# Kernel optimization log

Measured on AMD Instinct MI355X. Metric: run time of the kernel, lower is better.

Reference implementation:

```python
import jax, jax.numpy as jnp
import numpy as np

N_NODES = 100_000
N_EDGES = 1_000_000
D_X = 8
H = 128
N_DOM = 32768
N_BND = 8192
RE = 1.0 / 1.45e-05  # Reynolds number used in momentum residuals


def setup_inputs() -> dict:
    key = jax.random.key(0)
    ks = jax.random.split(key, 16)
    s = 0.05
    return {
        "x": jax.random.normal(ks[0], (N_NODES, D_X), jnp.float32),
        "x_mask": jax.random.uniform(ks[1], (N_NODES, 6), dtype=jnp.float32),
        "edge_index": jax.random.randint(ks[2], (2, N_EDGES), 0, N_NODES),
        "edge_attr": jax.random.normal(ks[3], (N_EDGES, 4), jnp.float32),
        "pos": jax.random.normal(ks[4], (N_NODES, 3), jnp.float32),
        "batch": jnp.zeros((N_NODES,), jnp.int32),
        "domain_sampling_points": jax.random.normal(ks[5], (N_DOM, 2), jnp.float32),
        "boundary_sampling_points": jax.random.normal(ks[6], (N_BND, 2), jnp.float32),
        "idxs_boundary_sampled": jax.random.randint(ks[7], (N_BND,), 0, N_NODES),
        # surrogate net parameters
        "Wx": jax.random.normal(ks[8], (D_X, H), jnp.float32) * s,
        "Wp": jax.random.normal(ks[9], (2, H), jnp.float32) * s,
        "We": jax.random.normal(ks[10], (3, H), jnp.float32) * s,
        "Wout": jax.random.normal(ks[11], (H, 3), jnp.float32) * s,
        "W1": jax.random.normal(ks[12], (2 + H, H), jnp.float32) * s,
        "b1": jnp.zeros((H,), jnp.float32),
        "W2": jax.random.normal(ks[13], (H, H), jnp.float32) * s,
        "b2": jnp.zeros((H,), jnp.float32),
        "W3": jax.random.normal(ks[14], (H, 3), jnp.float32) * s,
    }


def reference(x, x_mask, edge_index, edge_attr, pos, batch,
              domain_sampling_points, boundary_sampling_points,
              idxs_boundary_sampled,
              Wx, Wp, We, Wout, W1, b1, W2, b2, W3):
    pos2 = pos[:, :2]                              # pos = pos[:, :2]
    ea = edge_attr[:, jnp.array([0, 1, 3])]        # edge_attr[:, [0,1,3]]

    # --- surrogate GNN: one message-passing layer -> supervised output ---
    node_h = jnp.tanh(x @ Wx + pos2 @ Wp)          # [N, H]
    src, dst = edge_index[0], edge_index[1]
    msg = node_h[src] * (ea @ We)                  # [E, H] large gather (memory-bound)
    agg = jax.ops.segment_sum(msg, dst, num_segments=node_h.shape[0])
    h = jnp.tanh(node_h + agg)                     # [N, H]
    out_sup = h @ Wout                             # [N, 3]
    ctx = h.mean(axis=0)                           # [H] pooled graph context (constant wrt sp)

    # --- per-point coordinate network (u, v, p) ---
    def f_samp(sp):
        z = jnp.concatenate([sp, ctx])
        h1 = jnp.tanh(z @ W1 + b1)
        h2 = jnp.tanh(h1 @ W2 + b2)
        return h2 @ W3                             # [3] -> (u, v, p)

    sp = jnp.concatenate([domain_sampling_points, boundary_sampling_points])  # [S, 2]
    out_samp = jax.vmap(f_samp)(sp)                            # [S, 3]
    grads = jax.vmap(jax.jacrev(f_samp))(sp)                   # [S, 3, 2]
    hess = jax.vmap(jax.jacrev(jax.jacrev(f_samp)))(sp)        # [S, 3, 2, 2]

    nd = domain_sampling_points.shape[0]
    # --- domain (full_laminar) residuals ---
    u, v = out_samp[:nd, 0], out_samp[:nd, 1]
    u_x, u_y = grads[:nd, 0, 0], grads[:nd, 0, 1]
    v_x, v_y = grads[:nd, 1, 0], grads[:nd, 1, 1]
    p_x, p_y = grads[:nd, 2, 0], grads[:nd, 2, 1]
    u_xx, u_yy = hess[:nd, 0, 0, 0], hess[:nd, 0, 1, 1]
    v_xx, v_yy = hess[:nd, 1, 0, 0], hess[:nd, 1, 1, 1]
    continuity = u_x + v_y
    momentum_x = u * u_x + v * u_y + p_x - (u_xx + u_yy) / RE
    momentum_y = u * v_x + v * v_y + p_y - (v_xx + v_yy) / RE

    # --- boundary-condition residuals (vmapped BC math) ---
    bu, bv, bp = out_samp[nd:, 0], out_samp[nd:, 1], out_samp[nd:, 2]
    bu_x, bv_y = grads[nd:, 0, 0], grads[nd:, 1, 1]
    bp_x, bp_y = grads[nd:, 2, 0], grads[nd:, 2, 1]
    x_BC = x[idxs_boundary_sampled]                # [B, D_X]
    m = x_mask[idxs_boundary_sampled]              # [B, 6]
    t_x, t_y = x_BC[:, 0], x_BC[:, 1]
    n_x, n_y = -t_y, t_x
    r_vt = jnp.abs(t_x * bu + t_y * bv - x_BC[:, 2]) * m[:, 1]
    r_vn = jnp.abs(n_x * bu + n_y * bv - x_BC[:, 3]) * m[:, 2]
    r_p = jnp.abs(bp - x_BC[:, 4]) * m[:, 3]
    r_dvdn = jnp.abs(n_x * bu_x + n_y * bv_y - x_BC[:, 5]) * m[:, 4]
    r_dpdn = jnp.abs(n_x * bp_x + n_y * bp_y - x_BC[:, 6]) * m[:, 5]
    c = m[:, 1:6].sum(axis=1)
    boundary = (r_vt + r_vn + r_p + r_dvdn + r_dpdn) / c

    return (out_sup, continuity, momentum_x, momentum_y, boundary)
```

## Files before the change

kernel.cpp:

```cpp
#include <hip/hip_runtime.h>
#include <hip/hip_fp8.h>
#include <math.h>

#define H 128
#define DXI 8
#define NNODES 100000
#define NEDGES 1000000
#define NRUNS (NEDGES / 64)
#define NDOM 32768
#define NBND 8192
#define NPTS (NDOM + NBND)
#define INV_RE 1.45e-05f
#define NODE_BLOCKS 1024
#define NPR (NNODES / 8)

#define NSB ((NNODES + 1023) / 1024)

#define CONT_OFF (NNODES * 3)
#define MOMX_OFF (CONT_OFF + NDOM)
#define MOMY_OFF (MOMX_OFF + NDOM)
#define BND_OFF  (MOMY_OFF + NDOM)

#define KPAD 136
#define A_STRIDE (32 * KPAD)

typedef __attribute__((ext_vector_type(8))) short short8;
typedef __attribute__((ext_vector_type(4))) float f32x4;

__device__ __forceinline__ float fast_tanh(float x) {
    const float e = __builtin_amdgcn_exp2f(x * 2.88539008f);
    return fmaf(-2.f, __builtin_amdgcn_rcpf(e + 1.f), 1.f);
}

__device__ __forceinline__ unsigned pack_bf16(float a, float b) {
    unsigned ua = __float_as_uint(a), ub = __float_as_uint(b);
    ua += 0x7fffu + ((ua >> 16) & 1u);
    ub += 0x7fffu + ((ub >> 16) & 1u);
    return (ua >> 16) | (ub & 0xffff0000u);
}

__device__ __forceinline__ short to_bf16(float f) {
    unsigned u = __float_as_uint(f);
    u += 0x7fffu + ((u >> 16) & 1u);
    return (short)(u >> 16);
}

__device__ __forceinline__ float fp8_dec(unsigned b) {
    __hip_fp8_e4m3 d;
    d.__x = (__hip_fp8_storage_t)b;
    return (float)d;
}

__global__ __launch_bounds__(256) void hist_kernel(
    const int* __restrict__ eidx, int* __restrict__ counts)
{
    const int* dst = eidx + NEDGES;
    for (int e = blockIdx.x * 256 + threadIdx.x; e < NEDGES; e += gridDim.x * 256)
        atomicAdd(&counts[dst[e]], 1);
}

__global__ __launch_bounds__(256) void scan1_kernel(
    const int* __restrict__ counts, int* __restrict__ excl, int* __restrict__ bsum,
    const float* __restrict__ x, const float* __restrict__ pos,
    const float* __restrict__ Wx, const float* __restrict__ Wp,
    unsigned short* __restrict__ th, uint4* __restrict__ agg4)
{
    const int tid = threadIdx.x;

    if (blockIdx.x < NSB) {
        const int b = blockIdx.x;
        const int base = b * 1024 + tid * 4;
        int v0 = 0, v1 = 0, v2 = 0, v3 = 0;
        if (base + 3 < NNODES) {
            const int4 t = *(const int4*)(counts + base);
            v0 = t.x; v1 = t.y; v2 = t.z; v3 = t.w;
        } else {
            if (base     < NNODES) v0 = counts[base];
            if (base + 1 < NNODES) v1 = counts[base + 1];
            if (base + 2 < NNODES) v2 = counts[base + 2];
            if (base + 3 < NNODES) v3 = counts[base + 3];
        }
        const int own = v0 + v1 + v2 + v3;
        int s = own;
        const int lane = tid & 63, wv = tid >> 6;
#pragma unroll
        for (int d = 1; d < 64; d <<= 1) {
            const int t = __shfl_up(s, d);
            if (lane >= d) s += t;
        }
        __shared__ int wsum[4];
        if (lane == 63) wsum[wv] = s;
        __syncthreads();
        int woff = 0;
        for (int w = 0; w < wv; ++w) woff += wsum[w];
        const int e0 = s - own + woff;
        const int e1 = e0 + v0, e2 = e1 + v1, e3 = e2 + v2;
        if (base + 3 < NNODES) {
            *(int4*)(excl + base) = make_int4(e0, e1, e2, e3);
        } else {
            if (base     < NNODES) excl[base]     = e0;
            if (base + 1 < NNODES) excl[base + 1] = e1;
            if (base + 2 < NNODES) excl[base + 2] = e2;
            if (base + 3 < NNODES) excl[base + 3] = e3;
        }
        if (tid == 0) bsum[b] = wsum[0] + wsum[1] + wsum[2] + wsum[3];
    }

    const int gid = blockIdx.x * 256 + tid;
    const uint4 z = make_uint4(0u, 0u, 0u, 0u);
    for (size_t i = gid; i < (size_t)NNODES * 16; i += (size_t)gridDim.x * 256)
        agg4[i] = z;

    const int lane = tid & 63;
    const int wv   = tid >> 6;
    const int c0 = lane * 2, c1 = c0 + 1;
    float wxa[DXI], wxb_[DXI];
#pragma unroll
    for (int k = 0; k < DXI; ++k) { wxa[k] = Wx[k * H + c0]; wxb_[k] = Wx[k * H + c1]; }
    const float wp00 = Wp[c0], wp01 = Wp[H + c0];
    const float wp10 = Wp[c1], wp11 = Wp[H + c1];

    for (int n = blockIdx.x * 4 + wv; n < NNODES; n += gridDim.x * 4) {
        const float* xr = x + (size_t)n * DXI;
        const float px = pos[(size_t)n * 3], py = pos[(size_t)n * 3 + 1];
        float a0 = fmaf(wp00, px, wp01 * py);
        float a1 = fmaf(wp10, px, wp11 * py);
#pragma unroll
        for (int k = 0; k < DXI; ++k) {
            const float xv = xr[k];
            a0 = fmaf(xv, wxa[k], a0);
            a1 = fmaf(xv, wxb_[k], a1);
        }
        const __hip_fp8_e4m3 q0(fast_tanh(a0));
        const __hip_fp8_e4m3 q1(fast_tanh(a1));
        th[(size_t)n * 64 + lane] =
            (unsigned short)((unsigned)q0.__x | ((unsigned)q1.__x << 8));
    }
}

__global__ __launch_bounds__(128) void scan2_kernel(int* __restrict__ bsum)
{
    const int tid = threadIdx.x;
    int v = (tid < NSB) ? bsum[tid] : 0;
    const int own = v;
    const int lane = tid & 63, wv = tid >> 6;
#pragma unroll
    for (int d = 1; d < 64; d <<= 1) {
        const int t = __shfl_up(v, d);
        if (lane >= d) v += t;
    }
    __shared__ int ws2[2];
    if (lane == 63) ws2[wv] = v;
    __syncthreads();
    if (wv == 1) v += ws2[0];
    if (tid < NSB) bsum[tid] = v - own;
}

__global__ __launch_bounds__(256) void scan3_kernel(
    int* __restrict__ offsets, int* __restrict__ cursor, const int* __restrict__ bsum)
{
    const int tid = threadIdx.x, b = blockIdx.x;
    const int base = b * 1024 + tid * 4;
    const int add = bsum[b];
    if (base + 3 < NNODES) {
        int4 t = *(const int4*)(offsets + base);
        t.x += add; t.y += add; t.z += add; t.w += add;
        *(int4*)(offsets + base) = t;
        *(int4*)(cursor + base) = t;
    } else {
        for (int i = 0; i < 4; ++i)
            if (base + i < NNODES) {
                const int t = offsets[base + i] + add;
                offsets[base + i] = t;
                cursor[base + i] = t;
            }
    }
}

__global__ __launch_bounds__(256) void scatter_kernel(
    const int* __restrict__ eidx, const float* __restrict__ eattr,
    int* __restrict__ cursor, uint2* __restrict__ csrE)
{
    const int* dst = eidx + NEDGES;
    const int G   = gridDim.x >> 3;
    const int g   = blockIdx.x >> 3;
    const int r   = blockIdx.x & 7;
    const int dlo = r * NPR, dhi = dlo + NPR;
    for (int e = g * 256 + threadIdx.x; e < NEDGES; e += G * 256) {
        const int d = dst[e];
        if (d >= dlo && d < dhi) {
            const float4 ea = ((const float4*)eattr)[e];
            const int slot = atomicAdd(&cursor[d], 1);
            const __hip_fp8_e4m3 f0(ea.x), f1(ea.y), f3(ea.w);
            const unsigned long long v =
                (unsigned long long)(unsigned)eidx[e]
              | ((unsigned long long)(unsigned)d << 17)
              | ((unsigned long long)f0.__x << 34)
              | ((unsigned long long)f1.__x << 42)
              | ((unsigned long long)f3.__x << 50);
            csrE[slot] = make_uint2((unsigned)v, (unsigned)(v >> 32));
        }
    }
}

__global__ __launch_bounds__(256) void seg_edge_kernel(
    const uint2* __restrict__ csrE, const unsigned short* __restrict__ th,
    const float* __restrict__ We, unsigned* __restrict__ agg)
{
    const int run = blockIdx.x * 4 + (threadIdx.x >> 6);
    if (run >= NRUNS) return;
    const int lane = threadIdx.x & 63;
    const int c0 = lane * 2, c1 = c0 + 1;

    const float wea0 = We[c0], wea1 = We[H + c0], wea2 = We[2 * H + c0];
    const float web0 = We[c1], web1 = We[H + c1], web2 = We[2 * H + c1];

    const uint2 rec = csrE[(size_t)run * 64 + lane];
    const int mysrc = (int)(rec.x & 0x1FFFFu);
    const int mydst = (int)((rec.x >> 17) | ((rec.y & 3u) << 15));

    float acc0 = 0.f, acc1 = 0.f;
    bool first = true;
    int cur = __builtin_amdgcn_readlane(mydst, 0);

#pragma unroll
    for (int sub = 0; sub < 4; ++sub) {
        unsigned short rowv[16];
#pragma unroll
        for (int t = 0; t < 16; ++t) {
            const int s = __builtin_amdgcn_readlane(mysrc, sub * 16 + t);
            rowv[t] = th[(size_t)s * 64 + lane];
        }
#pragma unroll
        for (int t = 0; t < 16; ++t) {
            const int e = sub * 16 + t;
            const unsigned hi = (unsigned)__builtin_amdgcn_readlane((int)rec.y, e);
            const float e0f = fp8_dec((hi >> 2) & 0xffu);
            const float e1f = fp8_dec((hi >> 10) & 0xffu);
            const float e3f = fp8_dec((hi >> 18) & 0xffu);
            const float th0 = fp8_dec(rowv[t] & 0xffu);
            const float th1 = fp8_dec((unsigned)rowv[t] >> 8);
            const float w0 = fmaf(e0f, wea0, fmaf(e1f, wea1, e3f * wea2));
            const float w1 = fmaf(e0f, web0, fmaf(e1f, web1, e3f * web2));
            acc0 = fmaf(th0, w0, acc0);
            acc1 = fmaf(th1, w1, acc1);

            const int nxt = (e < 63) ? __builtin_amdgcn_readlane(mydst, e + 1) : -1;
            if (nxt != cur) {
                unsigned* p = agg + (size_t)cur * 64 + lane;
                if (first || e == 63) {
                    unsigned old = *p;
                    while (true) {
                        const float g0 = __uint_as_float(old << 16) + acc0;
                        const float g1 = __uint_as_float(old & 0xffff0000u) + acc1;
                        const unsigned nw = pack_bf16(g0, g1);
                        const unsigned prev = atomicCAS(p, old, nw);
                        if (prev == old) break;
                        old = prev;
                    }
                } else {
                    *p = pack_bf16(acc0, acc1);
                }
                acc0 = 0.f; acc1 = 0.f;
                first = false;
                cur = nxt;
            }
        }
    }
}

__global__ __launch_bounds__(256) void node_kernel(
    const float* __restrict__ x, const float* __restrict__ pos,
    const unsigned* __restrict__ agg,
    const float* __restrict__ Wx, const float* __restrict__ Wp,
    const float* __restrict__ Wout,
    float* __restrict__ out_sup, float* __restrict__ ctx_part)
{
    const int lane = threadIdx.x & 63;
    const int wv   = threadIdx.x >> 6;
    const int c0 = lane * 2, c1 = c0 + 1;

    float wxa[DXI], wxb_[DXI];
#pragma unroll
    for (int k = 0; k < DXI; ++k) { wxa[k] = Wx[k * H + c0]; wxb_[k] = Wx[k * H + c1]; }
    const float wp00 = Wp[c0], wp01 = Wp[H + c0];
    const float wp10 = Wp[c1], wp11 = Wp[H + c1];
    const float woa0 = Wout[c0 * 3], woa1 = Wout[c0 * 3 + 1], woa2 = Wout[c0 * 3 + 2];
    const float wob0 = Wout[c1 * 3], wob1 = Wout[c1 * 3 + 1], wob2 = Wout[c1 * 3 + 2];

    float ctx0 = 0.f, ctx1 = 0.f;

    for (int n = blockIdx.x * 4 + wv; n < NNODES; n += gridDim.x * 4) {
        const unsigned ag = agg[(size_t)n * 64 + lane];
        const float* xr = x + (size_t)n * DXI;
        const float px = pos[(size_t)n * 3], py = pos[(size_t)n * 3 + 1];
        float a0 = fmaf(wp00, px, wp01 * py);
        float a1 = fmaf(wp10, px, wp11 * py);
#pragma unroll
        for (int k = 0; k < DXI; ++k) {
            const float xv = xr[k];
            a0 = fmaf(xv, wxa[k], a0);
            a1 = fmaf(xv, wxb_[k], a1);
        }
        const float h0 = fast_tanh(fast_tanh(a0) + __uint_as_float(ag << 16));
        const float h1 = fast_tanh(fast_tanh(a1) + __uint_as_float(ag & 0xffff0000u));
        ctx0 += h0; ctx1 += h1;

        float p0 = fmaf(h0, woa0, h1 * wob0);
        float p1 = fmaf(h0, woa1, h1 * wob1);
        float p2 = fmaf(h0, woa2, h1 * wob2);
#pragma unroll
        for (int m = 32; m; m >>= 1) {
            p0 += __shfl_xor(p0, m);
            p1 += __shfl_xor(p1, m);
            p2 += __shfl_xor(p2, m);
        }
        if (lane == 0) {
            out_sup[(size_t)n * 3 + 0] = p0;
            out_sup[(size_t)n * 3 + 1] = p1;
            out_sup[(size_t)n * 3 + 2] = p2;
        }
    }

    __shared__ float part[4][H];
    part[wv][c0] = ctx0;
    part[wv][c1] = ctx1;
    __syncthreads();
    if (threadIdx.x < H) {
        const int ch = threadIdx.x;
        ctx_part[(size_t)blockIdx.x * H + ch] =
            part[0][ch] + part[1][ch] + part[2][ch] + part[3][ch];
    }
}

__global__ __launch_bounds__(128) void ctx_kernel(
    const float* __restrict__ ctx_part, const float* __restrict__ W1,
    const float* __restrict__ b1, float* __restrict__ tab)
{
    __shared__ float ctx[H];
    const int ch = threadIdx.x;
    float s0 = 0.f, s1 = 0.f, s2 = 0.f, s3 = 0.f;
#pragma unroll 4
    for (int b = 0; b < NODE_BLOCKS; b += 4) {
        s0 += ctx_part[(size_t)(b + 0) * H + ch];
        s1 += ctx_part[(size_t)(b + 1) * H + ch];
        s2 += ctx_part[(size_t)(b + 2) * H + ch];
        s3 += ctx_part[(size_t)(b + 3) * H + ch];
    }
    ctx[ch] = (s0 + s1 + s2 + s3) * (1.0f / (float)NNODES);
    __syncthreads();
    float acc = b1[ch];
    for (int k = 0; k < H; ++k) acc = fmaf(ctx[k], W1[(size_t)(2 + k) * H + ch], acc);
    const float A0 = W1[ch], A1 = W1[H + ch];
    tab[ch * 8 + 0] = A0;
    tab[ch * 8 + 1] = A1;
    tab[ch * 8 + 2] = acc;
    tab[ch * 8 + 3] = A0 * A0;
    tab[ch * 8 + 4] = A1 * A1;
    tab[ch * 8 + 5] = 0.f;
    tab[ch * 8 + 6] = 0.f;
    tab[ch * 8 + 7] = 0.f;
}

__global__ __launch_bounds__(256, 2) void samp_mfma_kernel(
    const float* __restrict__ dom, const float* __restrict__ bnd,
    const int* __restrict__ bidx,
    const float* __restrict__ x, const float* __restrict__ xmask,
    const float* __restrict__ tab,
    const float* __restrict__ W2, const float* __restrict__ b2,
    const float* __restrict__ W3, float* __restrict__ out)
{
    __shared__ __attribute__((aligned(16))) short Bt[128 * KPAD];
    __shared__ __attribute__((aligned(16))) short Alds[5 * A_STRIDE];
    __shared__ __attribute__((aligned(16))) float red[32][13];

    const int tid = threadIdx.x;
    const int blk = blockIdx.x;

    for (int i = tid; i < H * H; i += 256) {
        const int k = i >> 7, n = i & 127;
        Bt[n * KPAD + k] = to_bf16(W2[i]);
    }

    for (int idx = tid; idx < 32 * 64; idx += 256) {
        const int pl = idx >> 6;
        const int k0 = (idx & 63) * 2;
        const int p  = blk * 32 + pl;
        float spx, spy;
        if (p < NDOM) { spx = dom[(size_t)p * 2];          spy = dom[(size_t)p * 2 + 1]; }
        else          { spx = bnd[(size_t)(p - NDOM) * 2]; spy = bnd[(size_t)(p - NDOM) * 2 + 1]; }
        float v[2][5];
#pragma unroll
        for (int kk = 0; kk < 2; ++kk) {
            const int k = k0 + kk;
            const float4 t4 = *(const float4*)(tab + (size_t)k * 8);
            const float A1s = tab[(size_t)k * 8 + 4];
            const float A0 = t4.x, A1 = t4.y, cc = t4.z, A0s = t4.w;
            const float a1 = fmaf(spx, A0, fmaf(spy, A1, cc));
            const float e  = __builtin_amdgcn_exp2f(a1 * 2.88539008f);
            const float h1 = fmaf(-2.f, __builtin_amdgcn_rcpf(e + 1.f), 1.f);
            const float t1 = fmaf(-h1, h1, 1.f);
            const float m2 = -2.f * h1 * t1;
            v[kk][0] = h1;
            v[kk][1] = t1 * A0;
            v[kk][2] = t1 * A1;
            v[kk][3] = m2 * A0s;
            v[kk][4] = m2 * A1s;
        }
        const int base = pl * KPAD + k0;
#pragma unroll
        for (int q = 0; q < 5; ++q)
            *(unsigned*)&Alds[q * A_STRIDE + base] = pack_bf16(v[0][q], v[1][q]);
    }
    __syncthreads();

    const int lane = tid & 63;
    const int wv = tid >> 6;
    const int pt = wv >> 1;
    const int jh = wv & 1;
    const int ln = lane & 15;
    const int hi = lane >> 4;

    f32x4 acc[4][5];
#pragma unroll
    for (int nt = 0; nt < 4; ++nt)
#pragma unroll
        for (int q = 0; q < 5; ++q)
            acc[nt][q] = (f32x4){0.f, 0.f, 0.f, 0.f};

#pragma unroll
    for (int kc = 0; kc < 4; ++kc) {
        short8 af[5];
#pragma unroll
        for (int q = 0; q < 5; ++q)
            af[q] = *(const short8*)&Alds[q * A_STRIDE + (pt * 16 + ln) * KPAD + kc * 32 + hi * 8];
        short8 bfr[4];
#pragma unroll
        for (int nt = 0; nt < 4; ++nt)
            bfr[nt] = *(const short8*)&Bt[(jh * 64 + nt * 16 + ln) * KPAD + kc * 32 + hi * 8];
#pragma unroll
        for (int nt = 0; nt < 4; ++nt)
#pragma unroll
            for (int q = 0; q < 5; ++q)
                acc[nt][q] = __builtin_amdgcn_mfma_f32_16x16x32_bf16(af[q], bfr[nt], acc[nt][q], 0, 0, 0);
    }

    float w30[4], w31[4], w32[4], b2j[4];
#pragma unroll
    for (int nt = 0; nt < 4; ++nt) {
        const int j = jh * 64 + nt * 16 + ln;
        w30[nt] = W3[j * 3];
        w31[nt] = W3[j * 3 + 1];
        w32[nt] = W3[j * 3 + 2];
        b2j[nt] = b2[j];
    }

    float rr[4][13];
#pragma unroll
    for (int i = 0; i < 4; ++i)
#pragma unroll
        for (int c = 0; c < 13; ++c) rr[i][c] = 0.f;

#pragma unroll
    for (int i = 0; i < 4; ++i) {
#pragma unroll
        for (int nt = 0; nt < 4; ++nt) {
            const float a2v  = acc[nt][0][i] + b2j[nt];
            const float d2xv = acc[nt][1][i];
            const float d2yv = acc[nt][2][i];
            const float exxv = acc[nt][3][i];
            const float eyyv = acc[nt][4][i];
            const float h2 = fast_tanh(a2v);
            const float t2 = fmaf(-h2, h2, 1.f);
            const float gx = t2 * d2xv;
            const float gy = t2 * d2yv;
            const float hxx = fmaf(-2.f * h2 * gx, d2xv, t2 * exxv);
            const float hyy = fmaf(-2.f * h2 * gy, d2yv, t2 * eyyv);
            rr[i][0]  = fmaf(h2, w30[nt], rr[i][0]);
            rr[i][1]  = fmaf(h2, w31[nt], rr[i][1]);
            rr[i][2]  = fmaf(h2, w32[nt], rr[i][2]);
            rr[i][3]  = fmaf(gx, w30[nt], rr[i][3]);
            rr[i][4]  = fmaf(gx, w31[nt], rr[i][4]);
            rr[i][5]  = fmaf(gx, w32[nt], rr[i][5]);
            rr[i][6]  = fmaf(gy, w30[nt], rr[i][6]);
            rr[i][7]  = fmaf(gy, w31[nt], rr[i][7]);
            rr[i][8]  = fmaf(gy, w32[nt], rr[i][8]);
            rr[i][9]  = fmaf(hxx, w30[nt], rr[i][9]);
            rr[i][10] = fmaf(hxx, w31[nt], rr[i][10]);
            rr[i][11] = fmaf(hyy, w30[nt], rr[i][11]);
            rr[i][12] = fmaf(hyy, w31[nt], rr[i][12]);
        }
    }

#pragma unroll
    for (int m = 1; m < 16; m <<= 1)
#pragma unroll
        for (int i = 0; i < 4; ++i)
#pragma unroll
            for (int c = 0; c < 13; ++c)
                rr[i][c] += __shfl_xor(rr[i][c], m);

    if (ln == 0 && jh == 0) {
#pragma unroll
        for (int i = 0; i < 4; ++i) {
            const int pl = pt * 16 + hi * 4 + i;
#pragma unroll
            for (int c = 0; c < 13; ++c) red[pl][c] = rr[i][c];
        }
    }
    __syncthreads();
    if (ln == 0 && jh == 1) {
#pragma unroll
        for (int i = 0; i < 4; ++i) {
            const int pl = pt * 16 + hi * 4 + i;
#pragma unroll
            for (int c = 0; c < 13; ++c) red[pl][c] += rr[i][c];
        }
    }
    __syncthreads();

    if (tid < 32) {
        const int p = blk * 32 + tid;
        float s[13];
#pragma unroll
        for (int c = 0; c < 13; ++c) s[c] = red[tid][c];
        const float u = s[0], v = s[1], pp = s[2];
        const float ux = s[3], vx = s[4], px = s[5];
        const float uy = s[6], vy = s[7], py = s[8];
        const float uxx = s[9], vxx = s[10], uyy = s[11], vyy = s[12];
        if (p < NDOM) {
            out[CONT_OFF + p] = ux + vy;
            out[MOMX_OFF + p] = fmaf(u, ux, fmaf(v, uy, px)) - (uxx + uyy) * INV_RE;
            out[MOMY_OFF + p] = fmaf(u, vx, fmaf(v, vy, py)) - (vxx + vyy) * INV_RE;
        } else {
            const int i = p - NDOM;
            const int idx = bidx[i];
            const float* xbp = x + (size_t)idx * DXI;
            const float* mm = xmask + (size_t)idx * 6;
            const float tx = xbp[0], ty = xbp[1];
            const float nx = -ty, ny = tx;
            const float r_vt = fabsf(tx * u + ty * v - xbp[2]) * mm[1];
            const float r_vn = fabsf(nx * u + ny * v - xbp[3]) * mm[2];
            const float r_p  = fabsf(pp - xbp[4]) * mm[3];
            const float r_dv = fabsf(nx * ux + ny * vy - xbp[5]) * mm[4];
            const float r_dp = fabsf(nx * px + ny * py - xbp[6]) * mm[5];
            const float c = mm[1] + mm[2] + mm[3] + mm[4] + mm[5];
            out[BND_OFF + i] = (r_vt + r_vn + r_p + r_dv + r_dp) / c;
        }
    }
}

extern "C" void kernel_launch(void* const* d_in, const int* in_sizes, int n_in,
                              void* d_out, int out_size, void* d_ws, size_t ws_size,
                              hipStream_t stream) {
    const float* x     = (const float*)d_in[0];
    const float* xmask = (const float*)d_in[1];
    const int*   eidx  = (const int*)d_in[2];
    const float* eattr = (const float*)d_in[3];
    const float* pos   = (const float*)d_in[4];
    const float* dom   = (const float*)d_in[6];
    const float* bnd   = (const float*)d_in[7];
    const int*   bidx  = (const int*)d_in[8];
    const float* Wx    = (const float*)d_in[9];
    const float* Wp    = (const float*)d_in[10];
    const float* We    = (const float*)d_in[11];
    const float* Wout  = (const float*)d_in[12];
    const float* W1    = (const float*)d_in[13];
    const float* b1    = (const float*)d_in[14];
    const float* W2    = (const float*)d_in[15];
    const float* b2    = (const float*)d_in[16];
    const float* W3    = (const float*)d_in[17];

    float* out = (float*)d_out;

    int*            counts   = (int*)d_ws;
    int*            offsets  = counts + NNODES;
    int*            cursor   = offsets + NNODES + 8;
    int*            bsum     = cursor + NNODES;
    uint2*          csrE     = (uint2*)(bsum + 128);
    unsigned short* th       = (unsigned short*)(csrE + NEDGES);
    unsigned*       agg      = (unsigned*)(th + (size_t)NNODES * 64);
    float*          ctx_part = (float*)(agg + (size_t)NNODES * 64);
    float*          tab      = ctx_part + (size_t)NODE_BLOCKS * H;

    (void)hipMemsetAsync(counts, 0, (size_t)NNODES * sizeof(int), stream);

    hist_kernel<<<1024, 256, 0, stream>>>(eidx, counts);
    scan1_kernel<<<2048, 256, 0, stream>>>(counts, offsets, bsum, x, pos, Wx, Wp, th, (uint4*)agg);
    scan2_kernel<<<1, 128, 0, stream>>>(bsum);
    scan3_kernel<<<NSB, 256, 0, stream>>>(offsets, cursor, bsum);
    scatter_kernel<<<8192, 256, 0, stream>>>(eidx, eattr, cursor, csrE);
    seg_edge_kernel<<<(NRUNS + 3) / 4, 256, 0, stream>>>(csrE, th, We, agg);
    node_kernel<<<NODE_BLOCKS, 256, 0, stream>>>(x, pos, agg, Wx, Wp, Wout, out, ctx_part);
    ctx_kernel<<<1, H, 0, stream>>>(ctx_part, W1, b1, tab);
    samp_mfma_kernel<<<NPTS / 32, 256, 0, stream>>>(dom, bnd, bidx, x, xmask, tab, W2, b2, W3, out);
}
```

Baseline: 253.8 us.

## Pre-bucket packed edges by destination range in histogram pass before CSR scatter

The histogram kernel now also packs each edge record (src, dst, fp8 edge attrs) and writes it into one of 8 destination-range buckets, using block-local counters and a global bucket cursor. The scatter kernel then reads only its own bucket's packed records instead of having each of 8 range-groups rescan all edge indices and attributes. This removes the 8x redundant reading of dst and eattr in the old scatter. In exchange it adds an extra intermediate buffer write and read plus several block barriers per chunk in the histogram pass, and bucket capacity is fixed at RCAP per range.

```diff
diff --git a/kernel.cpp b/kernel.cpp
--- a/kernel.cpp
+++ b/kernel.cpp
@@ -13,6 +13,7 @@
 #define INV_RE 1.45e-05f
 #define NODE_BLOCKS 1024
 #define NPR (NNODES / 8)
+#define RCAP 131072
 
 #define NSB ((NNODES + 1023) / 1024)
 
@@ -51,12 +52,45 @@
     return (float)d;
 }
 
-__global__ __launch_bounds__(256) void hist_kernel(
-    const int* __restrict__ eidx, int* __restrict__ counts)
-{
+__global__ __launch_bounds__(256) void bucket_hist_kernel(
+    const int* __restrict__ eidx, const float* __restrict__ eattr,
+    int* __restrict__ counts, int* __restrict__ gcur, uint2* __restrict__ epack)
+{
+    __shared__ int lcnt[8];
+    __shared__ int lbase[8];
     const int* dst = eidx + NEDGES;
-    for (int e = blockIdx.x * 256 + threadIdx.x; e < NEDGES; e += gridDim.x * 256)
-        atomicAdd(&counts[dst[e]], 1);
+    const int CH = 1024;
+    const int ebeg = blockIdx.x * CH;
+#pragma unroll
+    for (int it = 0; it < CH / 256; ++it) {
+        const int e = ebeg + it * 256 + threadIdx.x;
+        if (threadIdx.x < 8) lcnt[threadIdx.x] = 0;
+        __syncthreads();
+        int r = -1, myoff = 0;
+        uint2 v = make_uint2(0u, 0u);
+        if (e < NEDGES) {
+            const int d = dst[e];
+            atomicAdd(&counts[d], 1);
+            const float4 ea = ((const float4*)eattr)[e];
+            const __hip_fp8_e4m3 f0(ea.x), f1(ea.y), f3(ea.w);
+            const unsigned long long pv =
+                (unsigned long long)(unsigned)eidx[e]
+              | ((unsigned long long)(unsigned)d << 17)
+              | ((unsigned long long)f0.__x << 34)
+              | ((unsigned long long)f1.__x << 42)
+              | ((unsigned long long)f3.__x << 50);
+            v = make_uint2((unsigned)pv, (unsigned)(pv >> 32));
+            r = d / NPR;
+            myoff = atomicAdd(&lcnt[r], 1);
+        }
+        __syncthreads();
+        if (threadIdx.x < 8)
+            lbase[threadIdx.x] = atomicAdd(&gcur[threadIdx.x], lcnt[threadIdx.x]);
+        __syncthreads();
+        if (r >= 0)
+            epack[(size_t)r * RCAP + lbase[r] + myoff] = v;
+        __syncthreads();
+    }
 }
 
 __global__ __launch_bounds__(256) void scan1_kernel(
@@ -177,29 +211,19 @@
     }
 }
 
-__global__ __launch_bounds__(256) void scatter_kernel(
-    const int* __restrict__ eidx, const float* __restrict__ eattr,
+__global__ __launch_bounds__(256) void scatter2_kernel(
+    const uint2* __restrict__ epack, const int* __restrict__ gcur,
     int* __restrict__ cursor, uint2* __restrict__ csrE)
 {
-    const int* dst = eidx + NEDGES;
-    const int G   = gridDim.x >> 3;
-    const int g   = blockIdx.x >> 3;
-    const int r   = blockIdx.x & 7;
-    const int dlo = r * NPR, dhi = dlo + NPR;
-    for (int e = g * 256 + threadIdx.x; e < NEDGES; e += G * 256) {
-        const int d = dst[e];
-        if (d >= dlo && d < dhi) {
-            const float4 ea = ((const float4*)eattr)[e];
-            const int slot = atomicAdd(&cursor[d], 1);
-            const __hip_fp8_e4m3 f0(ea.x), f1(ea.y), f3(ea.w);
-            const unsigned long long v =
-                (unsigned long long)(unsigned)eidx[e]
-              | ((unsigned long long)(unsigned)d << 17)
-              | ((unsigned long long)f0.__x << 34)
-              | ((unsigned long long)f1.__x << 42)
-              | ((unsigned long long)f3.__x << 50);
-            csrE[slot] = make_uint2((unsigned)v, (unsigned)(v >> 32));
-        }
+    const int r = blockIdx.x & 7;
+    const int g = blockIdx.x >> 3;
+    const int G = gridDim.x >> 3;
+    const int rcnt = gcur[r];
+    for (int i = g * 256 + threadIdx.x; i < rcnt; i += G * 256) {
+        const uint2 v = epack[(size_t)r * RCAP + i];
+        const int d = (int)((v.x >> 17) | ((v.y & 3u) << 15));
+        const int slot = atomicAdd(&cursor[d], 1);
+        csrE[slot] = v;
     }
 }
 
@@ -574,22 +598,24 @@
     float* out = (float*)d_out;
 
     int*            counts   = (int*)d_ws;
-    int*            offsets  = counts + NNODES;
+    int*            gcur     = counts + NNODES;
+    int*            offsets  = gcur + 8;
     int*            cursor   = offsets + NNODES + 8;
     int*            bsum     = cursor + NNODES;
     uint2*          csrE     = (uint2*)(bsum + 128);
-    unsigned short* th       = (unsigned short*)(csrE + NEDGES);
+    uint2*          epack    = csrE + NEDGES;
+    unsigned short* th       = (unsigned short*)(epack + 8 * RCAP);
     unsigned*       agg      = (unsigned*)(th + (size_t)NNODES * 64);
     float*          ctx_part = (float*)(agg + (size_t)NNODES * 64);
     float*          tab      = ctx_part + (size_t)NODE_BLOCKS * H;
 
-    (void)hipMemsetAsync(counts, 0, (size_t)NNODES * sizeof(int), stream);
-
-    hist_kernel<<<1024, 256, 0, stream>>>(eidx, counts);
+    (void)hipMemsetAsync(counts, 0, (size_t)(NNODES + 8) * sizeof(int), stream);
+
+    bucket_hist_kernel<<<(NEDGES + 1023) / 1024, 256, 0, stream>>>(eidx, eattr, counts, gcur, epack);
     scan1_kernel<<<2048, 256, 0, stream>>>(counts, offsets, bsum, x, pos, Wx, Wp, th, (uint4*)agg);
     scan2_kernel<<<1, 128, 0, stream>>>(bsum);
     scan3_kernel<<<NSB, 256, 0, stream>>>(offsets, cursor, bsum);
-    scatter_kernel<<<8192, 256, 0, stream>>>(eidx, eattr, cursor, csrE);
+    scatter2_kernel<<<4096, 256, 0, stream>>>(epack, gcur, cursor, csrE);
     seg_edge_kernel<<<(NRUNS + 3) / 4, 256, 0, stream>>>(csrE, th, We, agg);
     node_kernel<<<NODE_BLOCKS, 256, 0, stream>>>(x, pos, agg, Wx, Wp, Wout, out, ctx_part);
     ctx_kernel<<<1, H, 0, stream>>>(ctx_part, W1, b1, tab);
```

Result: slower. 273.4 us (+7.8%).
